# Kernel optimization log

Measured on AMD Instinct MI355X. Metric: run time of the kernel, lower is better.

Reference implementation:

```python
import jax, jax.numpy as jnp
import numpy as np

N = 100000   # nodes
E = 300000   # directed edges (avg degree 3, molecular graphs)
G = 4000     # molecules in the batch
IN = 9
HID = 128
HEADS = 4
NEG_SLOPE = 0.2


def setup_inputs() -> dict:
    key = jax.random.key(0)
    ks = jax.random.split(key, 12)
    x = jax.random.normal(ks[0], (N, IN), dtype=jnp.float32)
    edge_index = jax.random.randint(ks[1], (2, E), 0, N, dtype=jnp.int32)
    batch = jnp.sort(jax.random.randint(ks[2], (N,), 0, G, dtype=jnp.int32))
    s = 0.1  # keep activations in a sane range
    W1 = jax.random.normal(ks[3], (IN, HEADS * HID), dtype=jnp.float32) * s
    a_src1 = jax.random.normal(ks[4], (HEADS, HID), dtype=jnp.float32) * s
    a_dst1 = jax.random.normal(ks[5], (HEADS, HID), dtype=jnp.float32) * s
    b1 = jax.random.normal(ks[6], (HEADS * HID,), dtype=jnp.float32) * s
    W2 = jax.random.normal(ks[7], (HEADS * HID, HID), dtype=jnp.float32) * s
    a_src2 = jax.random.normal(ks[8], (1, HID), dtype=jnp.float32) * s
    a_dst2 = jax.random.normal(ks[9], (1, HID), dtype=jnp.float32) * s
    b2 = jax.random.normal(ks[10], (HID,), dtype=jnp.float32) * s
    return {"x": x, "edge_index": edge_index, "batch": batch,
            "W1": W1, "a_src1": a_src1, "a_dst1": a_dst1, "b1": b1,
            "W2": W2, "a_src2": a_src2, "a_dst2": a_dst2, "b2": b2}


def _gat_conv(x, edge_index, W, a_src, a_dst, b, heads, out_ch, concat):
    """PyG GATConv: linear proj, per-edge leaky-relu attention logits,
    segment softmax over destination nodes, scatter-add aggregation.
    add_self_loops=True (PyG default)."""
    n = x.shape[0]
    loops = jnp.arange(n, dtype=edge_index.dtype)
    src = jnp.concatenate([edge_index[0], loops])
    dst = jnp.concatenate([edge_index[1], loops])

    h = (x @ W).reshape(n, heads, out_ch)                  # [N, H, C]
    alpha_s = jnp.einsum('nhc,hc->nh', h, a_src)           # [N, H]
    alpha_d = jnp.einsum('nhc,hc->nh', h, a_dst)           # [N, H]

    logits = jax.nn.leaky_relu(alpha_s[src] + alpha_d[dst], NEG_SLOPE)  # [Etot, H]
    # numerically stable segment softmax over incoming edges of each dst
    m = jax.ops.segment_max(logits, dst, num_segments=n)   # [N, H] (finite: self-loops)
    e = jnp.exp(logits - m[dst])
    z = jax.ops.segment_sum(e, dst, num_segments=n)
    alpha = e / (z[dst] + 1e-16)                           # [Etot, H]

    msg = h[src] * alpha[:, :, None]                       # [Etot, H, C]
    out = jax.ops.segment_sum(msg, dst, num_segments=n)    # [N, H, C]
    if concat:
        out = out.reshape(n, heads * out_ch)
    else:
        out = out.mean(axis=1)
    return out + b


def reference(x, edge_index, batch, W1, a_src1, a_dst1, b1, W2, a_src2, a_dst2, b2):
    h = jax.nn.elu(_gat_conv(x, edge_index, W1, a_src1, a_dst1, b1, HEADS, HID, True))
    h = jax.nn.elu(_gat_conv(h, edge_index, W2, a_src2, a_dst2, b2, 1, HID, True))
    # global mean pool per graph
    sums = jax.ops.segment_sum(h, batch, num_segments=G)   # [G, HID]
    cnt = jax.ops.segment_sum(jnp.ones((h.shape[0],), h.dtype), batch, num_segments=G)
    return sums / jnp.maximum(cnt, 1.0)[:, None]
```

## Files before the change

kernel.cpp:

```cpp
#include <hip/hip_runtime.h>

#define N_NODES 100000
#define N_EDGES 300000
#define N_GRAPHS 4000
#define CAP 32

typedef float f32x4 __attribute__((ext_vector_type(4)));
typedef float f32x16 __attribute__((ext_vector_type(16)));
typedef __bf16 bf16x8 __attribute__((ext_vector_type(8)));
typedef __bf16 bf16x4 __attribute__((ext_vector_type(4)));
typedef __bf16 bf16x2 __attribute__((ext_vector_type(2)));
typedef _Float16 f16x8 __attribute__((ext_vector_type(8)));

static const size_t OFF_XA    = 0;
static const size_t OFF_AD4   = OFF_XA + (size_t)N_NODES * 16;
static const size_t OFF_P2B   = OFF_AD4 + (size_t)N_NODES * 4;
static const size_t OFF_ASAD2 = OFF_P2B + (size_t)N_NODES * 64;
static const size_t OFF_WSB   = OFF_ASAD2 + (size_t)N_NODES * 2;
static const size_t OFF_W1B   = OFF_WSB + 32768;
static const size_t OFF_GST   = OFF_W1B + 4096;
static const size_t OFF_INT   = OFF_GST + 4096;

#define PRE_NODE_END 391
#define PRE_PACKB_END 455
#define PRE_W1B_END 487
#define PRE_GST_END 503
#define PRE_BKT_END 1675

__device__ __forceinline__ float lrelu(float x) { return x < 0.f ? 0.2f * x : x; }
__device__ __forceinline__ float elu(float x)   { return x > 0.f ? x : __expf(x) - 1.f; }

__global__ __launch_bounds__(256) void k_pre(
    const float* __restrict__ x, const float* __restrict__ W1,
    const float* __restrict__ a_src1, const float* __restrict__ a_dst1,
    const float* __restrict__ W2, const int* __restrict__ batch,
    const int* __restrict__ ei,
    float* __restrict__ xa, float* __restrict__ ad4,
    __bf16* __restrict__ wsB, _Float16* __restrict__ w1b,
    int* __restrict__ deg, int* __restrict__ bucket, int* __restrict__ gstart) {
    int b = blockIdx.x, tid = threadIdx.x;
    if (b < PRE_NODE_END) {
        __shared__ float wf[72];
        if (tid < 72) {
            int isd = tid / 36, r = tid % 36, k = r / 4, h = r % 4;
            const float* a = isd ? a_dst1 : a_src1;
            float s = 0.f;
            for (int c = 0; c < 128; c++) s += W1[k * 512 + h * 128 + c] * a[h * 128 + c];
            wf[tid] = s;
        }
        __syncthreads();
        int n = b * 256 + tid;
        if (n >= N_NODES) return;
        float xv[9];
#pragma unroll
        for (int k = 0; k < 9; k++) xv[k] = x[n * 9 + k];
        float as[4], ad[4];
#pragma unroll
        for (int h = 0; h < 4; h++) {
            float s = 0.f, d = 0.f;
#pragma unroll
            for (int k = 0; k < 9; k++) {
                s += xv[k] * wf[k * 4 + h];
                d += xv[k] * wf[36 + k * 4 + h];
            }
            as[h] = s; ad[h] = d;
        }
        f32x4* xp = (f32x4*)(xa + (size_t)n * 16);
        xp[0] = (f32x4){xv[0], xv[1], xv[2], xv[3]};
        xp[1] = (f32x4){xv[4], xv[5], xv[6], xv[7]};
        xp[2] = (f32x4){xv[8], as[0], as[1], as[2]};
        xp[3] = (f32x4){as[3], 0.f, 0.f, 0.f};
        *(f32x4*)(ad4 + (size_t)n * 4) = (f32x4){ad[0], ad[1], ad[2], ad[3]};
    } else if (b < PRE_PACKB_END) {
        int t = (b - PRE_NODE_END) * 256 + tid;
#pragma unroll
        for (int m = 0; m < 4; m++) {
            int idx = t * 4 + m;
            int k = idx >> 7, nn = idx & 127;
            wsB[(size_t)nn * 512 + k] = (__bf16)W2[(size_t)k * 128 + nn];
        }
    } else if (b < PRE_W1B_END) {
        int t = (b - PRE_PACKB_END) * 256 + tid;
        int j = t >> 4, k = t & 15;
        w1b[t] = (k < 9) ? (_Float16)W1[(size_t)k * 512 + j] : (_Float16)0.f;
    } else if (b < PRE_GST_END) {
        int g = (b - PRE_W1B_END) * 256 + tid;
        if (g > N_GRAPHS) return;
        int lo = 0, hi = N_NODES;
        while (lo < hi) { int mid = (lo + hi) >> 1; if (batch[mid] < g) lo = mid + 1; else hi = mid; }
        gstart[g] = lo;
    } else {
        int e = (b - PRE_GST_END) * 256 + tid;
        if (e >= N_EDGES) return;
        int s = ei[e], d = ei[N_EDGES + e];
        int slot = atomicAdd(&deg[d], 1);
        if (slot < CAP) bucket[d * CAP + slot] = s;
    }
}

__global__ __launch_bounds__(512, 6) void k_gemm(
    const float* __restrict__ xa, const float* __restrict__ ad4,
    const int* __restrict__ deg, const int* __restrict__ bucket,
    const _Float16* __restrict__ w1b, const float* __restrict__ b1,
    const __bf16* __restrict__ wsB,
    const float* __restrict__ a_src2, const float* __restrict__ a_dst2,
    __bf16* __restrict__ p2b, float* __restrict__ asad2) {
    __shared__ __bf16 As[64 * 128];
    __shared__ _Float16 AgF[4 * 64 * 24];
    float* red2 = (float*)AgF;
    const int tid = threadIdx.x;
    const int lane = tid & 63;
    const int w = tid >> 6;
    const int i = lane & 15;
    const int q = lane >> 4;
    const int m0 = blockIdx.x * 64;

    {
        const int r = tid >> 3, sub = tid & 7;
        const int n = m0 + r;
        float acc[4][9] = {};
        float z[4] = {};
        const bool valid = (n < N_NODES);
        if (valid) {
            f32x4 adv = *(const f32x4*)(ad4 + (size_t)n * 4);
            int dg = deg[n];
            if (dg > CAP) dg = CAP;
#define GATHER1(SRC) do {                                                    \
            const f32x4* xp_ = (const f32x4*)(xa + (size_t)(SRC) * 16);      \
            f32x4 v0 = xp_[0], v1 = xp_[1], v2 = xp_[2], v3 = xp_[3];        \
            float e0 = __expf(lrelu(v2.y + adv.x));                          \
            float e1 = __expf(lrelu(v2.z + adv.y));                          \
            float e2 = __expf(lrelu(v2.w + adv.z));                          \
            float e3 = __expf(lrelu(v3.x + adv.w));                          \
            z[0] += e0; z[1] += e1; z[2] += e2; z[3] += e3;                  \
            float xs[9] = {v0.x, v0.y, v0.z, v0.w, v1.x, v1.y, v1.z, v1.w, v2.x}; \
            _Pragma("unroll")                                                \
            for (int k = 0; k < 9; k++) {                                    \
                acc[0][k] += e0 * xs[k]; acc[1][k] += e1 * xs[k];            \
                acc[2][k] += e2 * xs[k]; acc[3][k] += e3 * xs[k];            \
            }                                                                \
        } while (0)
            if (sub == 7) GATHER1(n);
            for (int j = sub; j < dg; j += 8) GATHER1(bucket[n * CAP + j]);
#undef GATHER1
        }
#pragma unroll
        for (int off = 1; off < 8; off <<= 1) {
#pragma unroll
            for (int h = 0; h < 4; h++) {
                z[h] += __shfl_xor(z[h], off);
#pragma unroll
                for (int k = 0; k < 9; k++) acc[h][k] += __shfl_xor(acc[h][k], off);
            }
        }
        if (sub == 0) {
#pragma unroll
            for (int h = 0; h < 4; h++) {
                float inv = valid ? 1.f / z[h] : 0.f;
                f16x8 p0, p1;
#pragma unroll
                for (int k = 0; k < 8; k++) { p0[k] = (_Float16)(acc[h][k] * inv); p1[k] = (_Float16)0.f; }
                p1[0] = (_Float16)(acc[h][8] * inv);
                _Float16* dst = AgF + (size_t)(h * 64 + r) * 24;
                *(f16x8*)dst = p0;
                *(f16x8*)(dst + 8) = p1;
            }
        }
    }
    __syncthreads();

    f32x4 acc[4];
#pragma unroll
    for (int r = 0; r < 4; r++) acc[r] = (f32x4){0.f, 0.f, 0.f, 0.f};

    const __bf16* bcol = wsB + (size_t)(w * 16 + i) * 512 + q * 8;
    const int nt = w & 1, jt = w >> 1;
    const int l31 = lane & 31, qh = lane >> 5;
    const int ilw = lane & 15, hw = (lane >> 4) & 1;

#pragma unroll
    for (int pass = 0; pass < 4; pass++) {
        bf16x8 breg[4];
#pragma unroll
        for (int kc = 0; kc < 4; kc++)
            breg[kc] = *(const bf16x8*)(bcol + pass * 128 + kc * 32);

        {
            f16x8 av = *(const f16x8*)(w1b + ((size_t)(pass * 128 + jt * 32 + l31) * 16 + qh * 8));
            f16x8 bv = *(const f16x8*)&AgF[(size_t)(pass * 64 + nt * 32 + l31) * 24 + qh * 8];
            f32x16 cfr = (f32x16){0.f, 0.f, 0.f, 0.f, 0.f, 0.f, 0.f, 0.f,
                                  0.f, 0.f, 0.f, 0.f, 0.f, 0.f, 0.f, 0.f};
            cfr = __builtin_amdgcn_mfma_f32_32x32x16_f16(av, bv, cfr, 0, 0, 0);
#pragma unroll
            for (int r2 = 0; r2 < 4; r2++) {
                f32x4 b1v = *(const f32x4*)(b1 + pass * 128 + jt * 32 + r2 * 8 + qh * 4);
                bf16x4 pk;
#pragma unroll
                for (int m = 0; m < 4; m++) pk[m] = (__bf16)elu(cfr[r2 * 4 + m] + b1v[m]);
                *(bf16x4*)&As[(size_t)(((nt * 2 + hw) * 4 + jt) * 512 +
                                       (r2 * 16 + ilw) * 8 + qh * 4)] = pk;
            }
        }
        __syncthreads();

#pragma unroll
        for (int kc = 0; kc < 4; kc++) {
#pragma unroll
            for (int rt = 0; rt < 4; rt++) {
                bf16x8 af = *(const bf16x8*)&As[(rt * 4 + kc) * 512 + lane * 8];
                acc[rt] = __builtin_amdgcn_mfma_f32_16x16x32_bf16(af, breg[kc], acc[rt], 0, 0, 0);
            }
        }
        __syncthreads();
    }

    float as2 = a_src2[w * 16 + i];
    float ad2 = a_dst2[w * 16 + i];
#pragma unroll
    for (int rt = 0; rt < 4; rt++) {
#pragma unroll
        for (int qq = 0; qq < 4; qq++) {
            int r2 = rt * 16 + q * 4 + qq;
            float v = acc[rt][qq];
            if (m0 + r2 < N_NODES)
                p2b[(size_t)(m0 + r2) * 128 + w * 16 + i] = (__bf16)v;
            float s = v * as2, d = v * ad2;
#pragma unroll
            for (int off = 1; off < 16; off <<= 1) {
                s += __shfl_xor(s, off);
                d += __shfl_xor(d, off);
            }
            if (i == 0) {
                red2[r2 * 16 + w * 2] = s;
                red2[r2 * 16 + w * 2 + 1] = d;
            }
        }
    }
    __syncthreads();
    if (tid < 128) {
        int r2 = tid >> 1, cc = tid & 1;
        float sum = 0.f;
#pragma unroll
        for (int ww = 0; ww < 8; ww++) sum += red2[r2 * 16 + ww * 2 + cc];
        if (m0 + r2 < N_NODES) asad2[(size_t)(m0 + r2) * 2 + cc] = sum;
    }
}

__global__ __launch_bounds__(256) void k_agg2pool(
    const __bf16* __restrict__ p2b, const float* __restrict__ asad2,
    const int* __restrict__ deg, const int* __restrict__ bucket,
    const float* __restrict__ b2, const int* __restrict__ gstart,
    float* __restrict__ out) {
    __shared__ float red[4 * 128];
    int g = blockIdx.x;
    int tid = threadIdx.x;
    int wv = __builtin_amdgcn_readfirstlane(tid >> 6);
    int lane = tid & 63;
    int s0n = gstart[g], e0n = gstart[g + 1];
    float b2a = b2[2 * lane], b2b = b2[2 * lane + 1];
    float g0 = 0.f, g1 = 0.f;
    for (int n = s0n + wv; n < e0n; n += 4) {
        float ad = asad2[n * 2 + 1];
        float e = __expf(lrelu(asad2[n * 2] + ad));
        float z = e;
        bf16x2 v = ((const bf16x2*)(p2b + (size_t)n * 128))[lane];
        float a0 = e * (float)v.x;
        float a1 = e * (float)v.y;
        int dg = deg[n];
        if (dg > CAP) dg = CAP;
        for (int j = 0; j < dg; j += 4) {
            int s0 = bucket[n * CAP + j];
            int s1 = bucket[n * CAP + min(j + 1, dg - 1)];
            int s2 = bucket[n * CAP + min(j + 2, dg - 1)];
            int s3 = bucket[n * CAP + min(j + 3, dg - 1)];
            float l0 = asad2[s0 * 2], l1 = asad2[s1 * 2];
            float l2 = asad2[s2 * 2], l3 = asad2[s3 * 2];
            bf16x2 w0 = ((const bf16x2*)(p2b + (size_t)s0 * 128))[lane];
            bf16x2 w1 = ((const bf16x2*)(p2b + (size_t)s1 * 128))[lane];
            bf16x2 w2 = ((const bf16x2*)(p2b + (size_t)s2 * 128))[lane];
            bf16x2 w3 = ((const bf16x2*)(p2b + (size_t)s3 * 128))[lane];
            float e0 = __expf(lrelu(l0 + ad));
            float e1 = (j + 1 < dg) ? __expf(lrelu(l1 + ad)) : 0.f;
            float e2 = (j + 2 < dg) ? __expf(lrelu(l2 + ad)) : 0.f;
            float e3 = (j + 3 < dg) ? __expf(lrelu(l3 + ad)) : 0.f;
            z += e0 + e1 + e2 + e3;
            a0 += e0 * (float)w0.x + e1 * (float)w1.x + e2 * (float)w2.x + e3 * (float)w3.x;
            a1 += e0 * (float)w0.y + e1 * (float)w1.y + e2 * (float)w2.y + e3 * (float)w3.y;
        }
        float inv = 1.f / z;
        g0 += elu(a0 * inv + b2a);
        g1 += elu(a1 * inv + b2b);
    }
    red[wv * 128 + 2 * lane] = g0;
    red[wv * 128 + 2 * lane + 1] = g1;
    __syncthreads();
    if (tid < 128) {
        float sum = red[tid] + red[128 + tid] + red[256 + tid] + red[384 + tid];
        int cnt = e0n - s0n;
        out[(size_t)g * 128 + tid] = sum / (float)(cnt > 0 ? cnt : 1);
    }
}

extern "C" void kernel_launch(void* const* d_in, const int* in_sizes, int n_in,
                              void* d_out, int out_size, void* d_ws, size_t ws_size,
                              hipStream_t stream) {
    const float* x       = (const float*)d_in[0];
    const int*   ei      = (const int*)d_in[1];
    const int*   batch   = (const int*)d_in[2];
    const float* W1      = (const float*)d_in[3];
    const float* a_src1  = (const float*)d_in[4];
    const float* a_dst1  = (const float*)d_in[5];
    const float* b1      = (const float*)d_in[6];
    const float* W2      = (const float*)d_in[7];
    const float* a_src2  = (const float*)d_in[8];
    const float* a_dst2  = (const float*)d_in[9];
    const float* b2      = (const float*)d_in[10];
    float* out = (float*)d_out;

    float* wsf   = (float*)d_ws;
    float* xa    = wsf + OFF_XA;
    float* ad4   = wsf + OFF_AD4;
    __bf16* p2b  = (__bf16*)(wsf + OFF_P2B);
    float* asad2 = wsf + OFF_ASAD2;
    __bf16* wsB  = (__bf16*)(wsf + OFF_WSB);
    _Float16* w1b = (_Float16*)(wsf + OFF_W1B);
    int* gstart  = (int*)(wsf + OFF_GST);
    int* wsi    = (int*)(wsf + OFF_INT);
    int* deg    = wsi;
    int* bucket = wsi + N_NODES;

    hipMemsetAsync(deg, 0, N_NODES * sizeof(int), stream);
    k_pre<<<PRE_BKT_END, 256, 0, stream>>>(x, W1, a_src1, a_dst1, W2, batch, ei,
                                           xa, ad4, wsB, w1b, deg, bucket, gstart);
    k_gemm<<<(N_NODES + 63) / 64, 512, 0, stream>>>(xa, ad4, deg, bucket, w1b, b1,
                                                    wsB, a_src2, a_dst2, p2b, asad2);
    k_agg2pool<<<N_GRAPHS, 256, 0, stream>>>(p2b, asad2, deg, bucket, b2, gstart, out);
}
```

Measured before the change: 213.0 us.

## Split layer-1 gather from GEMM into separate aggregation kernel

```diff
diff --git a/kernel.cpp b/kernel.cpp
--- a/kernel.cpp
+++ b/kernel.cpp
@@ -98,16 +98,76 @@
     }
 }
 
-__global__ __launch_bounds__(512, 6) void k_gemm(
+__global__ __launch_bounds__(256, 4) void k_agg1(
     const float* __restrict__ xa, const float* __restrict__ ad4,
     const int* __restrict__ deg, const int* __restrict__ bucket,
-    const _Float16* __restrict__ w1b, const float* __restrict__ b1,
-    const __bf16* __restrict__ wsB,
+    _Float16* __restrict__ agg) {
+    const int tid = threadIdx.x;
+    const int r = tid >> 2, sub = tid & 3;
+    const int n = blockIdx.x * 64 + r;
+    float acc[4][9] = {};
+    float z[4] = {};
+    if (n < N_NODES) {
+        const f32x4 adv = *(const f32x4*)(ad4 + (size_t)n * 4);
+        int dg = deg[n];
+        if (dg > CAP) dg = CAP;
+#define GATHER1(SRC) do {                                                    \
+        const f32x4* xp_ = (const f32x4*)(xa + (size_t)(SRC) * 16);          \
+        f32x4 v0 = xp_[0], v1 = xp_[1], v2 = xp_[2], v3 = xp_[3];            \
+        float e0 = __expf(lrelu(v2.y + adv.x));                              \
+        float e1 = __expf(lrelu(v2.z + adv.y));                              \
+        float e2 = __expf(lrelu(v2.w + adv.z));                              \
+        float e3 = __expf(lrelu(v3.x + adv.w));                              \
+        z[0] += e0; z[1] += e1; z[2] += e2; z[3] += e3;                      \
+        float xs[9] = {v0.x, v0.y, v0.z, v0.w, v1.x, v1.y, v1.z, v1.w, v2.x}; \
+        _Pragma("unroll")                                                    \
+        for (int k = 0; k < 9; k++) {                                        \
+            acc[0][k] += e0 * xs[k]; acc[1][k] += e1 * xs[k];                \
+            acc[2][k] += e2 * xs[k]; acc[3][k] += e3 * xs[k];                \
+        }                                                                    \
+    } while (0)
+        if (sub == 3) GATHER1(n);
+        int j = sub;
+        int srcn = (j < dg) ? bucket[n * CAP + j] : -1;
+        while (srcn >= 0) {
+            int src = srcn;
+            j += 4;
+            srcn = (j < dg) ? bucket[n * CAP + j] : -1;
+            GATHER1(src);
+        }
+#undef GATHER1
+    }
+#pragma unroll
+    for (int off = 1; off <= 2; off <<= 1) {
+#pragma unroll
+        for (int h = 0; h < 4; h++) {
+            z[h] += __shfl_xor(z[h], off);
+#pragma unroll
+            for (int k = 0; k < 9; k++) acc[h][k] += __shfl_xor(acc[h][k], off);
+        }
+    }
+    if (sub == 0 && n < N_NODES) {
+        _Float16* dst = agg + (size_t)n * 128;
+#pragma unroll
+        for (int h = 0; h < 4; h++) {
+            float inv = 1.f / z[h];
+            f16x8 p0, p1;
+#pragma unroll
+            for (int k = 0; k < 8; k++) { p0[k] = (_Float16)(acc[h][k] * inv); p1[k] = (_Float16)0.f; }
+            p1[0] = (_Float16)(acc[h][8] * inv);
+            *(f16x8*)(dst + h * 16) = p0;
+            *(f16x8*)(dst + h * 16 + 8) = p1;
+        }
+    }
+}
+
+__global__ __launch_bounds__(512, 6) void k_mm(
+    const _Float16* agg, const _Float16* __restrict__ w1b,
+    const float* __restrict__ b1, const __bf16* __restrict__ wsB,
     const float* __restrict__ a_src2, const float* __restrict__ a_dst2,
-    __bf16* __restrict__ p2b, float* __restrict__ asad2) {
+    __bf16* p2b, float* __restrict__ asad2) {
     __shared__ __bf16 As[64 * 128];
-    __shared__ _Float16 AgF[4 * 64 * 24];
-    float* red2 = (float*)AgF;
+    float* red2 = (float*)As;
     const int tid = threadIdx.x;
     const int lane = tid & 63;
     const int w = tid >> 6;
@@ -115,60 +175,6 @@
     const int q = lane >> 4;
     const int m0 = blockIdx.x * 64;
 
-    {
-        const int r = tid >> 3, sub = tid & 7;
-        const int n = m0 + r;
-        float acc[4][9] = {};
-        float z[4] = {};
-        const bool valid = (n < N_NODES);
-        if (valid) {
-            f32x4 adv = *(const f32x4*)(ad4 + (size_t)n * 4);
-            int dg = deg[n];
-            if (dg > CAP) dg = CAP;
-#define GATHER1(SRC) do {                                                    \
-            const f32x4* xp_ = (const f32x4*)(xa + (size_t)(SRC) * 16);      \
-            f32x4 v0 = xp_[0], v1 = xp_[1], v2 = xp_[2], v3 = xp_[3];        \
-            float e0 = __expf(lrelu(v2.y + adv.x));                          \
-            float e1 = __expf(lrelu(v2.z + adv.y));                          \
-            float e2 = __expf(lrelu(v2.w + adv.z));                          \
-            float e3 = __expf(lrelu(v3.x + adv.w));                          \
-            z[0] += e0; z[1] += e1; z[2] += e2; z[3] += e3;                  \
-            float xs[9] = {v0.x, v0.y, v0.z, v0.w, v1.x, v1.y, v1.z, v1.w, v2.x}; \
-            _Pragma("unroll")                                                \
-            for (int k = 0; k < 9; k++) {                                    \
-                acc[0][k] += e0 * xs[k]; acc[1][k] += e1 * xs[k];            \
-                acc[2][k] += e2 * xs[k]; acc[3][k] += e3 * xs[k];            \
-            }                                                                \
-        } while (0)
-            if (sub == 7) GATHER1(n);
-            for (int j = sub; j < dg; j += 8) GATHER1(bucket[n * CAP + j]);
-#undef GATHER1
-        }
-#pragma unroll
-        for (int off = 1; off < 8; off <<= 1) {
-#pragma unroll
-            for (int h = 0; h < 4; h++) {
-                z[h] += __shfl_xor(z[h], off);
-#pragma unroll
-                for (int k = 0; k < 9; k++) acc[h][k] += __shfl_xor(acc[h][k], off);
-            }
-        }
-        if (sub == 0) {
-#pragma unroll
-            for (int h = 0; h < 4; h++) {
-                float inv = valid ? 1.f / z[h] : 0.f;
-                f16x8 p0, p1;
-#pragma unroll
-                for (int k = 0; k < 8; k++) { p0[k] = (_Float16)(acc[h][k] * inv); p1[k] = (_Float16)0.f; }
-                p1[0] = (_Float16)(acc[h][8] * inv);
-                _Float16* dst = AgF + (size_t)(h * 64 + r) * 24;
-                *(f16x8*)dst = p0;
-                *(f16x8*)(dst + 8) = p1;
-            }
-        }
-    }
-    __syncthreads();
-
     f32x4 acc[4];
 #pragma unroll
     for (int r = 0; r < 4; r++) acc[r] = (f32x4){0.f, 0.f, 0.f, 0.f};
@@ -177,6 +183,7 @@
     const int nt = w & 1, jt = w >> 1;
     const int l31 = lane & 31, qh = lane >> 5;
     const int ilw = lane & 15, hw = (lane >> 4) & 1;
+    const _Float16* agrow = agg + (size_t)(m0 + nt * 32 + l31) * 128 + qh * 8;
 
 #pragma unroll
     for (int pass = 0; pass < 4; pass++) {
@@ -187,7 +194,7 @@
 
         {
             f16x8 av = *(const f16x8*)(w1b + ((size_t)(pass * 128 + jt * 32 + l31) * 16 + qh * 8));
-            f16x8 bv = *(const f16x8*)&AgF[(size_t)(pass * 64 + nt * 32 + l31) * 24 + qh * 8];
+            f16x8 bv = *(const f16x8*)(agrow + pass * 16);
             f32x16 cfr = (f32x16){0.f, 0.f, 0.f, 0.f, 0.f, 0.f, 0.f, 0.f,
                                   0.f, 0.f, 0.f, 0.f, 0.f, 0.f, 0.f, 0.f};
             cfr = __builtin_amdgcn_mfma_f32_32x32x16_f16(av, bv, cfr, 0, 0, 0);
@@ -321,6 +328,7 @@
     float* xa    = wsf + OFF_XA;
     float* ad4   = wsf + OFF_AD4;
     __bf16* p2b  = (__bf16*)(wsf + OFF_P2B);
+    _Float16* agg = (_Float16*)p2b;
     float* asad2 = wsf + OFF_ASAD2;
     __bf16* wsB  = (__bf16*)(wsf + OFF_WSB);
     _Float16* w1b = (_Float16*)(wsf + OFF_W1B);
@@ -332,7 +340,8 @@
     hipMemsetAsync(deg, 0, N_NODES * sizeof(int), stream);
     k_pre<<<PRE_BKT_END, 256, 0, stream>>>(x, W1, a_src1, a_dst1, W2, batch, ei,
                                            xa, ad4, wsB, w1b, deg, bucket, gstart);
-    k_gemm<<<(N_NODES + 63) / 64, 512, 0, stream>>>(xa, ad4, deg, bucket, w1b, b1,
-                                                    wsB, a_src2, a_dst2, p2b, asad2);
+    k_agg1<<<(N_NODES + 63) / 64, 256, 0, stream>>>(xa, ad4, deg, bucket, agg);
+    k_mm<<<(N_NODES + 63) / 64, 512, 0, stream>>>(agg, w1b, b1, wsB,
+                                                  a_src2, a_dst2, p2b, asad2);
     k_agg2pool<<<N_GRAPHS, 256, 0, stream>>>(p2b, asad2, deg, bucket, b2, gstart, out);
 }
```

Result: faster. 202.8 us (-4.8%).
